# Kernel optimization log

Hardware: AMD Instinct MI355X
Metric: run time of the kernel (lower is better)

The kernel has to match this reference:

```python
import jax, jax.numpy as jnp
import numpy as np
import math

BS, SEQ, DIM, H, LK = 4, 4096, 768, 12, 256
HD = DIM // H  # 64
WIN = SEQ // LK  # 16, AdaptiveAvgPool1d reduces to uniform windows since SEQ % LK == 0


def setup_inputs() -> dict:
    key = jax.random.key(0)
    ks = jax.random.split(key, 12)
    s = 1.0 / math.sqrt(DIM)
    return {
        "query": jax.random.normal(ks[0], (BS, SEQ, DIM), jnp.float32),
        "key": jax.random.normal(ks[1], (BS, SEQ, DIM), jnp.float32),
        "value": jax.random.normal(ks[2], (BS, SEQ, DIM), jnp.float32),
        "mask": jax.random.normal(ks[3], (BS, SEQ), jnp.float32),  # mask<0 -> padded
        "Wq": jax.random.normal(ks[4], (DIM, DIM), jnp.float32) * s,
        "bq": jnp.zeros((DIM,), jnp.float32),
        "Wk": jax.random.normal(ks[5], (DIM, DIM), jnp.float32) * s,
        "bk": jnp.zeros((DIM,), jnp.float32),
        "Wv": jax.random.normal(ks[6], (DIM, DIM), jnp.float32) * s,
        "bv": jnp.zeros((DIM,), jnp.float32),
        "Wo": jax.random.normal(ks[7], (DIM, DIM), jnp.float32) * s,
        "bo": jnp.zeros((DIM,), jnp.float32),
    }


def reference(query, key, value, mask, Wq, bq, Wk, bk, Wv, bv, Wo, bo):
    bs, q_len, _ = query.shape
    # projections (nn.Linear: x @ W.T + b)
    Q = query @ Wq.T + bq
    K = key @ Wk.T + bk
    V = value @ Wv.T + bv
    # mask-fill padded K/V rows with 0 (mask dim==2 path: bool_mask = mask < 0)
    keep = (mask >= 0)[:, :, None]  # [bs, seq, 1]
    K = jnp.where(keep, K, 0.0)
    V = jnp.where(keep, V, 0.0)
    # adaptive avg pool over sequence -> linformer_k=256 (uniform windows of 16)
    Kc = K.reshape(bs, LK, WIN, DIM).mean(axis=2)  # [bs, 256, dim]
    Vc = V.reshape(bs, LK, WIN, DIM).mean(axis=2)
    # split heads
    Qh = Q.reshape(bs, q_len, H, HD) / math.sqrt(HD)  # scale fused
    Kh = Kc.reshape(bs, LK, H, HD)
    Vh = Vc.reshape(bs, LK, H, HD)
    # low-rank attention: [bs, h, q_len, 256]
    scores = jnp.einsum("bqhd,bkhd->bhqk", Qh, Kh)
    weights = jax.nn.softmax(scores, axis=-1)
    context = jnp.einsum("bhqk,bkhd->bqhd", weights, Vh).reshape(bs, q_len, DIM)
    return context @ Wo.T + bo
```

## Files before the change

### kernel.cpp

```cpp
#include <hip/hip_runtime.h>

#define BS_   4
#define SEQ_  4096
#define DIM_  768
#define NH_   12
#define HD_   64
#define LK_   256

typedef __attribute__((ext_vector_type(8))) short          bf8;
typedef __attribute__((ext_vector_type(8))) unsigned short us8;
typedef __attribute__((ext_vector_type(4))) float          f32x4;

typedef unsigned int u32g __attribute__((address_space(1)));
typedef unsigned int u32l __attribute__((address_space(3)));

#define LOG2E 1.44269504088896340736f

__device__ __forceinline__ unsigned short f2bf(float f) {
  unsigned u = __builtin_bit_cast(unsigned, f);
  u += 0x7fffu + ((u >> 16) & 1u);
  return (unsigned short)(u >> 16);
}

__device__ __forceinline__ us8 cvt8(const float* __restrict__ p) {
  const float4 a = *(const float4*)p;
  const float4 b = *(const float4*)(p + 4);
  us8 r;
  r[0] = f2bf(a.x); r[1] = f2bf(a.y); r[2] = f2bf(a.z); r[3] = f2bf(a.w);
  r[4] = f2bf(b.x); r[5] = f2bf(b.y); r[6] = f2bf(b.z); r[7] = f2bf(b.w);
  return r;
}

__global__ __launch_bounds__(256) void cvtbf_kernel(
    const float* __restrict__ query,
    const float* __restrict__ Wq, const float* __restrict__ Wk,
    const float* __restrict__ Wv, const float* __restrict__ Wo,
    unsigned short* __restrict__ Qbf, unsigned short* __restrict__ Wbf)
{
  const int i = blockIdx.x * 256 + threadIdx.x;
  const int QN8 = (BS_ * SEQ_ * DIM_) / 8;
  const int WN8 = (DIM_ * DIM_) / 8;
  if (i < QN8) { *(us8*)(Qbf + (size_t)i * 8) = cvt8(query + (size_t)i * 8); return; }
  int j = i - QN8;
  const float* src; unsigned short* dst;
  if      (j <     WN8) { src = Wq; dst = Wbf;                   }
  else if (j < 2 * WN8) { src = Wk; dst = Wbf + DIM_*DIM_;     j -=     WN8; }
  else if (j < 3 * WN8) { src = Wv; dst = Wbf + 2*DIM_*DIM_;   j -= 2 * WN8; }
  else if (j < 4 * WN8) { src = Wo; dst = Wbf + 3*DIM_*DIM_;   j -= 3 * WN8; }
  else return;
  *(us8*)(dst + (size_t)j * 8) = cvt8(src + (size_t)j * 8);
}

__global__ __launch_bounds__(256) void pool_kernel(
    const float* __restrict__ key, const float* __restrict__ value,
    const float* __restrict__ mask,
    unsigned short* __restrict__ pk, unsigned short* __restrict__ pv,
    float* __restrict__ frac)
{
  const int blk = blockIdx.x;
  const int b = blk >> 8;
  const int l = blk & 255;
  const int tid = threadIdx.x;
  __shared__ float keep[16];
  if (tid < 16) keep[tid] = (mask[b * SEQ_ + l * 16 + tid] >= 0.f) ? 1.f : 0.f;
  __syncthreads();
  float ak0 = 0.f, ak1 = 0.f, ak2 = 0.f, av0 = 0.f, av1 = 0.f, av2 = 0.f;
  #pragma unroll 1
  for (int w = 0; w < 16; ++w) {
    if (keep[w] != 0.f) {
      const size_t row = (size_t)(b * SEQ_ + l * 16 + w) * DIM_;
      const float* kr = key + row;
      const float* vr = value + row;
      ak0 += kr[tid]; ak1 += kr[tid + 256]; ak2 += kr[tid + 512];
      av0 += vr[tid]; av1 += vr[tid + 256]; av2 += vr[tid + 512];
    }
  }
  const size_t o = (size_t)(b * LK_ + l) * DIM_;
  const float s = 1.f / 16.f;
  pk[o + tid] = f2bf(ak0 * s); pk[o + tid + 256] = f2bf(ak1 * s); pk[o + tid + 512] = f2bf(ak2 * s);
  pv[o + tid] = f2bf(av0 * s); pv[o + tid + 256] = f2bf(av1 * s); pv[o + tid + 512] = f2bf(av2 * s);
  if (tid == 0) {
    float c = 0.f;
    for (int w = 0; w < 16; ++w) c += keep[w];
    frac[b * LK_ + l] = c * s;
  }
}

template<int SA, int SB, int MODE>
__global__ __launch_bounds__(256) void gemm_bt(
    const void* __restrict__ Aptr, const void* __restrict__ Bptr,
    const float* __restrict__ bias, const float* __restrict__ frac,
    void* __restrict__ Cout, int M, float scale)
{
  constexpr int K = DIM_;
  __shared__ __align__(16) unsigned short lA[128 * 32];
  __shared__ __align__(16) unsigned short lB[128 * 32];
  const int tid  = threadIdx.x;
  const int lane = tid & 63;
  const int wave = tid >> 6;
  const int brow = blockIdx.x * 128;
  const int bcol = blockIdx.y * 128;
  const int wr   = (wave >> 1) * 64;
  const int wc   = (wave & 1) * 64;
  const int fr   = lane & 15;
  const int fk   = (lane >> 4) * 8;

  f32x4 acc[4][4];
  #pragma unroll
  for (int i = 0; i < 4; ++i)
    #pragma unroll
    for (int j = 0; j < 4; ++j) acc[i][j] = (f32x4){0.f, 0.f, 0.f, 0.f};

  const int srow = tid >> 2;
  const int schk = (tid & 3) * 8;

  for (int k0 = 0; k0 < K; k0 += 32) {
    us8 a0, a1, b0, b1;
    if (SA == 1) {
      const float* A = (const float*)Aptr;
      a0 = cvt8(A + (size_t)(brow + srow) * K + k0 + schk);
      a1 = cvt8(A + (size_t)(brow + srow + 64) * K + k0 + schk);
    }
    if (SB == 1) {
      const float* B = (const float*)Bptr;
      b0 = cvt8(B + (size_t)(bcol + srow) * K + k0 + schk);
      b1 = cvt8(B + (size_t)(bcol + srow + 64) * K + k0 + schk);
    }
    __syncthreads();
    if (SA == 0) {
      const unsigned short* A = (const unsigned short*)Aptr;
      __builtin_amdgcn_global_load_lds(
          (const u32g*)(A + (size_t)(brow + srow) * K + k0 + schk),
          (u32l*)&lA[tid * 8], 16, 0, 0);
      __builtin_amdgcn_global_load_lds(
          (const u32g*)(A + (size_t)(brow + srow + 64) * K + k0 + schk),
          (u32l*)&lA[2048 + tid * 8], 16, 0, 0);
    } else {
      *(us8*)&lA[tid * 8]        = a0;
      *(us8*)&lA[2048 + tid * 8] = a1;
    }
    if (SB == 0) {
      const unsigned short* B = (const unsigned short*)Bptr;
      __builtin_amdgcn_global_load_lds(
          (const u32g*)(B + (size_t)(bcol + srow) * K + k0 + schk),
          (u32l*)&lB[tid * 8], 16, 0, 0);
      __builtin_amdgcn_global_load_lds(
          (const u32g*)(B + (size_t)(bcol + srow + 64) * K + k0 + schk),
          (u32l*)&lB[2048 + tid * 8], 16, 0, 0);
    } else {
      *(us8*)&lB[tid * 8]        = b0;
      *(us8*)&lB[2048 + tid * 8] = b1;
    }
    __syncthreads();
    bf8 af[4], bfv[4];
    #pragma unroll
    for (int mi = 0; mi < 4; ++mi)
      af[mi] = *(const bf8*)&lA[(wr + mi * 16 + fr) * 32 + fk];
    #pragma unroll
    for (int ni = 0; ni < 4; ++ni)
      bfv[ni] = *(const bf8*)&lB[(wc + ni * 16 + fr) * 32 + fk];
    #pragma unroll
    for (int mi = 0; mi < 4; ++mi)
      #pragma unroll
      for (int ni = 0; ni < 4; ++ni)
        acc[mi][ni] = __builtin_amdgcn_mfma_f32_16x16x32_bf16(af[mi], bfv[ni], acc[mi][ni], 0, 0, 0);
  }

  const int er = (lane >> 4) * 4;
  #pragma unroll
  for (int mi = 0; mi < 4; ++mi) {
    #pragma unroll
    for (int ni = 0; ni < 4; ++ni) {
      #pragma unroll
      for (int j = 0; j < 4; ++j) {
        const int r = brow + wr + mi * 16 + er + j;
        const int c = bcol + wc + ni * 16 + fr;
        float v = acc[mi][ni][j];
        if (MODE == 0) {
          v = (v + bias[c]) * scale;
          ((unsigned short*)Cout)[(size_t)r * DIM_ + c] = f2bf(v);
        } else if (MODE == 2) {
          ((float*)Cout)[(size_t)r * DIM_ + c] = v + bias[c];
        } else if (MODE == 3) {
          v += frac[r] * bias[c];
          const int bb = r >> 8, key = r & 255;
          const int hh = c >> 6, dd = c & 63;
          const int bh = bb * NH_ + hh;
          const size_t idx = (size_t)bh * 16384 +
              ((key >> 5) * 4 + (dd >> 4)) * 512 + ((key >> 3) & 3) * 128 +
              (dd & 15) * 8 + (key & 7);
          ((unsigned short*)Cout)[idx] = f2bf(v);
        } else {
          v += frac[r] * bias[c];
          const int bb = r >> 8, key = r & 255;
          const int hh = c >> 6, dd = c & 63;
          const int bh = bb * NH_ + hh;
          const int t = key >> 5, g = (key >> 3) & 3, sub = (key >> 2) & 1, jj = key & 3;
          const int frk = g * 4 + jj;
          const size_t idx = (size_t)bh * 16384 +
              (((t * 2 + sub) * 2) + (dd >> 5)) * 512 + ((dd >> 3) & 3) * 128 +
              frk * 8 + (dd & 7);
          ((unsigned short*)Cout)[idx] = f2bf(v);
        }
      }
    }
  }
}

__global__ __launch_bounds__(256) void attn_fused(
    const unsigned short* __restrict__ Qh,
    const unsigned short* __restrict__ Kf,
    const unsigned short* __restrict__ Vf,
    unsigned short* __restrict__ ctx)
{
  const int tid  = threadIdx.x;
  const int lane = tid & 63;
  const int wave = tid >> 6;
  const int bh = blockIdx.y;
  const int b = bh / NH_, h = bh % NH_;
  const int fr = lane & 15;
  const int hi = lane >> 4;
  const int qrow = blockIdx.x * 64 + wave * 16;

  const unsigned short* qp = Qh + (size_t)(b * SEQ_ + qrow + fr) * DIM_ + h * HD_ + hi * 8;
  const bf8 q0 = *(const bf8*)qp;
  const bf8 q1 = *(const bf8*)(qp + 32);

  const unsigned short* kb = Kf + (size_t)bh * 16384 + lane * 8;
  f32x4 scA[8], scB[8];
  #pragma unroll
  for (int s = 0; s < 8; ++s) {
    const bf8 ka0 = *(const bf8*)(kb + (s * 4 + 0) * 512);
    const bf8 ka1 = *(const bf8*)(kb + (s * 4 + 1) * 512);
    const bf8 kb0 = *(const bf8*)(kb + (s * 4 + 2) * 512);
    const bf8 kb1 = *(const bf8*)(kb + (s * 4 + 3) * 512);
    f32x4 x = (f32x4){0.f, 0.f, 0.f, 0.f};
    x = __builtin_amdgcn_mfma_f32_16x16x32_bf16(ka0, q0, x, 0, 0, 0);
    x = __builtin_amdgcn_mfma_f32_16x16x32_bf16(ka1, q1, x, 0, 0, 0);
    scA[s] = x;
    f32x4 y = (f32x4){0.f, 0.f, 0.f, 0.f};
    y = __builtin_amdgcn_mfma_f32_16x16x32_bf16(kb0, q0, y, 0, 0, 0);
    y = __builtin_amdgcn_mfma_f32_16x16x32_bf16(kb1, q1, y, 0, 0, 0);
    scB[s] = y;
  }

  float m = -1e30f;
  #pragma unroll
  for (int s = 0; s < 8; ++s)
    #pragma unroll
    for (int j = 0; j < 4; ++j) { m = fmaxf(m, scA[s][j]); m = fmaxf(m, scB[s][j]); }
  m = fmaxf(m, __shfl_xor(m, 16));
  m = fmaxf(m, __shfl_xor(m, 32));
  float sum = 0.f;
  #pragma unroll
  for (int s = 0; s < 8; ++s)
    #pragma unroll
    for (int j = 0; j < 4; ++j) {
      float pa = exp2f(scA[s][j] - m); scA[s][j] = pa; sum += pa;
      float pb = exp2f(scB[s][j] - m); scB[s][j] = pb; sum += pb;
    }
  sum += __shfl_xor(sum, 16);
  sum += __shfl_xor(sum, 32);
  const float inv = 1.f / sum;

  bf8 pa[8];
  #pragma unroll
  for (int s = 0; s < 8; ++s) {
    bf8 p;
    #pragma unroll
    for (int j = 0; j < 4; ++j) {
      p[j]     = (short)f2bf(scA[s][j] * inv);
      p[4 + j] = (short)f2bf(scB[s][j] * inv);
    }
    pa[s] = p;
  }

  const unsigned short* vb = Vf + (size_t)bh * 16384 + lane * 8;
  f32x4 acc[4];
  #pragma unroll
  for (int ct = 0; ct < 4; ++ct) acc[ct] = (f32x4){0.f, 0.f, 0.f, 0.f};
  #pragma unroll
  for (int s = 0; s < 8; ++s) {
    #pragma unroll
    for (int ct = 0; ct < 4; ++ct) {
      const bf8 vf = *(const bf8*)(vb + (s * 4 + ct) * 512);
      acc[ct] = __builtin_amdgcn_mfma_f32_16x16x32_bf16(pa[s], vf, acc[ct], 0, 0, 0);
    }
  }

  #pragma unroll
  for (int ct = 0; ct < 4; ++ct)
    #pragma unroll
    for (int j = 0; j < 4; ++j)
      ctx[(size_t)(b * SEQ_ + qrow + hi * 4 + j) * DIM_ + h * HD_ + ct * 16 + fr] =
          f2bf(acc[ct][j]);
}

extern "C" void kernel_launch(void* const* d_in, const int* in_sizes, int n_in,
                              void* d_out, int out_size, void* d_ws, size_t ws_size,
                              hipStream_t stream) {
  const float* query = (const float*)d_in[0];
  const float* key   = (const float*)d_in[1];
  const float* value = (const float*)d_in[2];
  const float* mask  = (const float*)d_in[3];
  const float* Wq    = (const float*)d_in[4];
  const float* bq    = (const float*)d_in[5];
  const float* Wk    = (const float*)d_in[6];
  const float* bk    = (const float*)d_in[7];
  const float* Wv    = (const float*)d_in[8];
  const float* bv    = (const float*)d_in[9];
  const float* Wo    = (const float*)d_in[10];
  const float* bo    = (const float*)d_in[11];
  float* out = (float*)d_out;

  char* ws = (char*)d_ws;
  unsigned short* Qh  = (unsigned short*)ws;
  unsigned short* ctx = (unsigned short*)(ws + 25165824);
  unsigned short* pK  = (unsigned short*)(ws + 50331648);
  unsigned short* pV  = (unsigned short*)(ws + 51904512);
  unsigned short* Kf  = (unsigned short*)(ws + 53477376);
  unsigned short* Vf  = (unsigned short*)(ws + 55050240);
  float*          frac = (float*)(ws + 56623104);
  unsigned short* Wbf = (unsigned short*)(ws + 56627200);
  const size_t NEED_BF = 56627200 + 4718592;

  const float qscale = 0.125f * LOG2E;

  pool_kernel<<<dim3(1024), dim3(256), 0, stream>>>(key, value, mask, pK, pV, frac);

  if (ws_size >= NEED_BF) {
    unsigned short* Qbf = ctx;
    cvtbf_kernel<<<dim3(7296), dim3(256), 0, stream>>>(query, Wq, Wk, Wv, Wo, Qbf, Wbf);
    gemm_bt<0, 0, 0><<<dim3(128, 6), dim3(256), 0, stream>>>(Qbf, Wbf,                 bq, nullptr, Qh, 16384, qscale);
    gemm_bt<0, 0, 4><<<dim3(8, 6),   dim3(256), 0, stream>>>(pK,  Wbf + DIM_*DIM_,     bk, frac,    Kf, 1024, 1.f);
    gemm_bt<0, 0, 3><<<dim3(8, 6),   dim3(256), 0, stream>>>(pV,  Wbf + 2*DIM_*DIM_,   bv, frac,    Vf, 1024, 1.f);
    attn_fused<<<dim3(64, 48), dim3(256), 0, stream>>>(Qh, Kf, Vf, ctx);
    gemm_bt<0, 0, 2><<<dim3(128, 6), dim3(256), 0, stream>>>(ctx, Wbf + 3*DIM_*DIM_,   bo, nullptr, out, 16384, 1.f);
  } else {
    gemm_bt<1, 1, 0><<<dim3(128, 6), dim3(256), 0, stream>>>(query, Wq, bq, nullptr, Qh, 16384, qscale);
    gemm_bt<0, 1, 4><<<dim3(8, 6),   dim3(256), 0, stream>>>(pK,    Wk, bk, frac,    Kf, 1024, 1.f);
    gemm_bt<0, 1, 3><<<dim3(8, 6),   dim3(256), 0, stream>>>(pV,    Wv, bv, frac,    Vf, 1024, 1.f);
    attn_fused<<<dim3(64, 48), dim3(256), 0, stream>>>(Qh, Kf, Vf, ctx);
    gemm_bt<0, 1, 2><<<dim3(128, 6), dim3(256), 0, stream>>>(ctx,   Wo, bo, nullptr, out, 16384, 1.f);
  }
}
```

Before: 155.4 us.

## Merge K/V projection launches, swizzle GEMM tiles, vectorize pooling, add MFMA priority hints

Several changes at once. The pooling kernel now uses 384 threads, each summing a float4 from either key or value, and writes packed bf16 stores. The K and V projection GEMMs are merged into one launch using blockIdx.z, which relies on pV and Vf sitting at fixed offsets after pK and Kf. The large GEMMs use a 1D grid with a block-index swizzle meant to improve L2 reuse. s_setprio hints are placed around the MFMA sections of attention, and the fp32-input fallback path is removed. These aim to cut launch count and memory inefficiency, but they depend on the workspace always being large enough.

```diff
diff --git a/kernel.cpp b/kernel.cpp
--- a/kernel.cpp
+++ b/kernel.cpp
@@ -9,6 +9,7 @@
 
 typedef __attribute__((ext_vector_type(8))) short          bf8;
 typedef __attribute__((ext_vector_type(8))) unsigned short us8;
+typedef __attribute__((ext_vector_type(4))) unsigned short us4;
 typedef __attribute__((ext_vector_type(4))) float          f32x4;
 
 typedef unsigned int u32g __attribute__((address_space(1)));
@@ -51,7 +52,7 @@
   *(us8*)(dst + (size_t)j * 8) = cvt8(src + (size_t)j * 8);
 }
 
-__global__ __launch_bounds__(256) void pool_kernel(
+__global__ __launch_bounds__(384) void pool_kernel(
     const float* __restrict__ key, const float* __restrict__ value,
     const float* __restrict__ mask,
     unsigned short* __restrict__ pk, unsigned short* __restrict__ pv,
@@ -64,33 +65,36 @@
   __shared__ float keep[16];
   if (tid < 16) keep[tid] = (mask[b * SEQ_ + l * 16 + tid] >= 0.f) ? 1.f : 0.f;
   __syncthreads();
-  float ak0 = 0.f, ak1 = 0.f, ak2 = 0.f, av0 = 0.f, av1 = 0.f, av2 = 0.f;
+  const int isV = tid >= 192;
+  const int c = isV ? tid - 192 : tid;
+  const float* src = isV ? value : key;
+  float4 acc = make_float4(0.f, 0.f, 0.f, 0.f);
   #pragma unroll 1
   for (int w = 0; w < 16; ++w) {
     if (keep[w] != 0.f) {
-      const size_t row = (size_t)(b * SEQ_ + l * 16 + w) * DIM_;
-      const float* kr = key + row;
-      const float* vr = value + row;
-      ak0 += kr[tid]; ak1 += kr[tid + 256]; ak2 += kr[tid + 512];
-      av0 += vr[tid]; av1 += vr[tid + 256]; av2 += vr[tid + 512];
-    }
-  }
-  const size_t o = (size_t)(b * LK_ + l) * DIM_;
+      const float4 v = *(const float4*)(src + (size_t)(b * SEQ_ + l * 16 + w) * DIM_ + c * 4);
+      acc.x += v.x; acc.y += v.y; acc.z += v.z; acc.w += v.w;
+    }
+  }
   const float s = 1.f / 16.f;
-  pk[o + tid] = f2bf(ak0 * s); pk[o + tid + 256] = f2bf(ak1 * s); pk[o + tid + 512] = f2bf(ak2 * s);
-  pv[o + tid] = f2bf(av0 * s); pv[o + tid + 256] = f2bf(av1 * s); pv[o + tid + 512] = f2bf(av2 * s);
+  unsigned short* dst = isV ? pv : pk;
+  us4 o4;
+  o4[0] = f2bf(acc.x * s); o4[1] = f2bf(acc.y * s);
+  o4[2] = f2bf(acc.z * s); o4[3] = f2bf(acc.w * s);
+  *(us4*)(dst + (size_t)(b * LK_ + l) * DIM_ + c * 4) = o4;
   if (tid == 0) {
-    float c = 0.f;
-    for (int w = 0; w < 16; ++w) c += keep[w];
-    frac[b * LK_ + l] = c * s;
-  }
-}
-
-template<int SA, int SB, int MODE>
+    float cnt = 0.f;
+    for (int w = 0; w < 16; ++w) cnt += keep[w];
+    frac[b * LK_ + l] = cnt * s;
+  }
+}
+
+template<int MODE, int SWZ>
 __global__ __launch_bounds__(256) void gemm_bt(
-    const void* __restrict__ Aptr, const void* __restrict__ Bptr,
-    const float* __restrict__ bias, const float* __restrict__ frac,
-    void* __restrict__ Cout, int M, float scale)
+    const void* __restrict__ Aptr_, const void* __restrict__ Bptr_,
+    const float* __restrict__ bias, const float* __restrict__ bias2,
+    const float* __restrict__ frac,
+    void* __restrict__ Cout, float scale)
 {
   constexpr int K = DIM_;
   __shared__ __align__(16) unsigned short lA[128 * 32];
@@ -98,8 +102,28 @@
   const int tid  = threadIdx.x;
   const int lane = tid & 63;
   const int wave = tid >> 6;
-  const int brow = blockIdx.x * 128;
-  const int bcol = blockIdx.y * 128;
+
+  int bx, by;
+  if (SWZ) {
+    const int r = (blockIdx.x & 7) * 96 + (blockIdx.x >> 3);
+    bx = r / 6; by = r % 6;
+  } else {
+    bx = blockIdx.x; by = blockIdx.y;
+  }
+  const int brow = bx * 128;
+  const int bcol = by * 128;
+
+  const unsigned short* A = (const unsigned short*)Aptr_;
+  const unsigned short* Bw = (const unsigned short*)Bptr_;
+  const float* bb = bias;
+  int isV = 0;
+  if (MODE == 34) {
+    isV = blockIdx.z;
+    A  += (size_t)isV * (BS_ * LK_ * DIM_);
+    Bw += (size_t)isV * (DIM_ * DIM_);
+    if (isV) bb = bias2;
+  }
+
   const int wr   = (wave >> 1) * 64;
   const int wc   = (wave & 1) * 64;
   const int fr   = lane & 15;
@@ -115,42 +139,19 @@
   const int schk = (tid & 3) * 8;
 
   for (int k0 = 0; k0 < K; k0 += 32) {
-    us8 a0, a1, b0, b1;
-    if (SA == 1) {
-      const float* A = (const float*)Aptr;
-      a0 = cvt8(A + (size_t)(brow + srow) * K + k0 + schk);
-      a1 = cvt8(A + (size_t)(brow + srow + 64) * K + k0 + schk);
-    }
-    if (SB == 1) {
-      const float* B = (const float*)Bptr;
-      b0 = cvt8(B + (size_t)(bcol + srow) * K + k0 + schk);
-      b1 = cvt8(B + (size_t)(bcol + srow + 64) * K + k0 + schk);
-    }
     __syncthreads();
-    if (SA == 0) {
-      const unsigned short* A = (const unsigned short*)Aptr;
-      __builtin_amdgcn_global_load_lds(
-          (const u32g*)(A + (size_t)(brow + srow) * K + k0 + schk),
-          (u32l*)&lA[tid * 8], 16, 0, 0);
-      __builtin_amdgcn_global_load_lds(
-          (const u32g*)(A + (size_t)(brow + srow + 64) * K + k0 + schk),
-          (u32l*)&lA[2048 + tid * 8], 16, 0, 0);
-    } else {
-      *(us8*)&lA[tid * 8]        = a0;
-      *(us8*)&lA[2048 + tid * 8] = a1;
-    }
-    if (SB == 0) {
-      const unsigned short* B = (const unsigned short*)Bptr;
-      __builtin_amdgcn_global_load_lds(
-          (const u32g*)(B + (size_t)(bcol + srow) * K + k0 + schk),
-          (u32l*)&lB[tid * 8], 16, 0, 0);
-      __builtin_amdgcn_global_load_lds(
-          (const u32g*)(B + (size_t)(bcol + srow + 64) * K + k0 + schk),
-          (u32l*)&lB[2048 + tid * 8], 16, 0, 0);
-    } else {
-      *(us8*)&lB[tid * 8]        = b0;
-      *(us8*)&lB[2048 + tid * 8] = b1;
-    }
+    __builtin_amdgcn_global_load_lds(
+        (const u32g*)(A + (size_t)(brow + srow) * K + k0 + schk),
+        (u32l*)&lA[tid * 8], 16, 0, 0);
+    __builtin_amdgcn_global_load_lds(
+        (const u32g*)(A + (size_t)(brow + srow + 64) * K + k0 + schk),
+        (u32l*)&lA[2048 + tid * 8], 16, 0, 0);
+    __builtin_amdgcn_global_load_lds(
+        (const u32g*)(Bw + (size_t)(bcol + srow) * K + k0 + schk),
+        (u32l*)&lB[tid * 8], 16, 0, 0);
+    __builtin_amdgcn_global_load_lds(
+        (const u32g*)(Bw + (size_t)(bcol + srow + 64) * K + k0 + schk),
+        (u32l*)&lB[2048 + tid * 8], 16, 0, 0);
     __syncthreads();
     bf8 af[4], bfv[4];
     #pragma unroll
@@ -181,25 +182,23 @@
           ((unsigned short*)Cout)[(size_t)r * DIM_ + c] = f2bf(v);
         } else if (MODE == 2) {
           ((float*)Cout)[(size_t)r * DIM_ + c] = v + bias[c];
-        } else if (MODE == 3) {
-          v += frac[r] * bias[c];
-          const int bb = r >> 8, key = r & 255;
+        } else {
+          v += frac[r] * bb[c];
+          const int bb_ = r >> 8, key = r & 255;
           const int hh = c >> 6, dd = c & 63;
-          const int bh = bb * NH_ + hh;
-          const size_t idx = (size_t)bh * 16384 +
-              ((key >> 5) * 4 + (dd >> 4)) * 512 + ((key >> 3) & 3) * 128 +
-              (dd & 15) * 8 + (key & 7);
-          ((unsigned short*)Cout)[idx] = f2bf(v);
-        } else {
-          v += frac[r] * bias[c];
-          const int bb = r >> 8, key = r & 255;
-          const int hh = c >> 6, dd = c & 63;
-          const int bh = bb * NH_ + hh;
-          const int t = key >> 5, g = (key >> 3) & 3, sub = (key >> 2) & 1, jj = key & 3;
-          const int frk = g * 4 + jj;
-          const size_t idx = (size_t)bh * 16384 +
-              (((t * 2 + sub) * 2) + (dd >> 5)) * 512 + ((dd >> 3) & 3) * 128 +
-              frk * 8 + (dd & 7);
+          const int bh = bb_ * NH_ + hh;
+          size_t idx;
+          if (isV) {
+            idx = (size_t)bh * 16384 +
+                ((key >> 5) * 4 + (dd >> 4)) * 512 + ((key >> 3) & 3) * 128 +
+                (dd & 15) * 8 + (key & 7) + 786432;
+          } else {
+            const int t = key >> 5, g = (key >> 3) & 3, sub = (key >> 2) & 1, jj = key & 3;
+            const int frk = g * 4 + jj;
+            idx = (size_t)bh * 16384 +
+                (((t * 2 + sub) * 2) + (dd >> 5)) * 512 + ((dd >> 3) & 3) * 128 +
+                frk * 8 + (dd & 7);
+          }
           ((unsigned short*)Cout)[idx] = f2bf(v);
         }
       }
@@ -228,6 +227,7 @@
 
   const unsigned short* kb = Kf + (size_t)bh * 16384 + lane * 8;
   f32x4 scA[8], scB[8];
+  __builtin_amdgcn_s_setprio(1);
   #pragma unroll
   for (int s = 0; s < 8; ++s) {
     const bf8 ka0 = *(const bf8*)(kb + (s * 4 + 0) * 512);
@@ -243,6 +243,7 @@
     y = __builtin_amdgcn_mfma_f32_16x16x32_bf16(kb1, q1, y, 0, 0, 0);
     scB[s] = y;
   }
+  __builtin_amdgcn_s_setprio(0);
 
   float m = -1e30f;
   #pragma unroll
@@ -256,8 +257,8 @@
   for (int s = 0; s < 8; ++s)
     #pragma unroll
     for (int j = 0; j < 4; ++j) {
-      float pa = exp2f(scA[s][j] - m); scA[s][j] = pa; sum += pa;
-      float pb = exp2f(scB[s][j] - m); scB[s][j] = pb; sum += pb;
+      const float pa = exp2f(scA[s][j] - m); scA[s][j] = pa; sum += pa;
+      const float pb = exp2f(scB[s][j] - m); scB[s][j] = pb; sum += pb;
     }
   sum += __shfl_xor(sum, 16);
   sum += __shfl_xor(sum, 32);
@@ -279,6 +280,7 @@
   f32x4 acc[4];
   #pragma unroll
   for (int ct = 0; ct < 4; ++ct) acc[ct] = (f32x4){0.f, 0.f, 0.f, 0.f};
+  __builtin_amdgcn_s_setprio(1);
   #pragma unroll
   for (int s = 0; s < 8; ++s) {
     #pragma unroll
@@ -287,6 +289,7 @@
       acc[ct] = __builtin_amdgcn_mfma_f32_16x16x32_bf16(pa[s], vf, acc[ct], 0, 0, 0);
     }
   }
+  __builtin_amdgcn_s_setprio(0);
 
   #pragma unroll
   for (int ct = 0; ct < 4; ++ct)
@@ -322,25 +325,17 @@
   unsigned short* Vf  = (unsigned short*)(ws + 55050240);
   float*          frac = (float*)(ws + 56623104);
   unsigned short* Wbf = (unsigned short*)(ws + 56627200);
-  const size_t NEED_BF = 56627200 + 4718592;
+  unsigned short* Qbf = ctx;
 
   const float qscale = 0.125f * LOG2E;
 
-  pool_kernel<<<dim3(1024), dim3(256), 0, stream>>>(key, value, mask, pK, pV, frac);
-
-  if (ws_size >= NEED_BF) {
-    unsigned short* Qbf = ctx;
-    cvtbf_kernel<<<dim3(7296), dim3(256), 0, stream>>>(query, Wq, Wk, Wv, Wo, Qbf, Wbf);
-    gemm_bt<0, 0, 0><<<dim3(128, 6), dim3(256), 0, stream>>>(Qbf, Wbf,                 bq, nullptr, Qh, 16384, qscale);
-    gemm_bt<0, 0, 4><<<dim3(8, 6),   dim3(256), 0, stream>>>(pK,  Wbf + DIM_*DIM_,     bk, frac,    Kf, 1024, 1.f);
-    gemm_bt<0, 0, 3><<<dim3(8, 6),   dim3(256), 0, stream>>>(pV,  Wbf + 2*DIM_*DIM_,   bv, frac,    Vf, 1024, 1.f);
-    attn_fused<<<dim3(64, 48), dim3(256), 0, stream>>>(Qh, Kf, Vf, ctx);
-    gemm_bt<0, 0, 2><<<dim3(128, 6), dim3(256), 0, stream>>>(ctx, Wbf + 3*DIM_*DIM_,   bo, nullptr, out, 16384, 1.f);
-  } else {
-    gemm_bt<1, 1, 0><<<dim3(128, 6), dim3(256), 0, stream>>>(query, Wq, bq, nullptr, Qh, 16384, qscale);
-    gemm_bt<0, 1, 4><<<dim3(8, 6),   dim3(256), 0, stream>>>(pK,    Wk, bk, frac,    Kf, 1024, 1.f);
-    gemm_bt<0, 1, 3><<<dim3(8, 6),   dim3(256), 0, stream>>>(pV,    Wv, bv, frac,    Vf, 1024, 1.f);
-    attn_fused<<<dim3(64, 48), dim3(256), 0, stream>>>(Qh, Kf, Vf, ctx);
-    gemm_bt<0, 1, 2><<<dim3(128, 6), dim3(256), 0, stream>>>(ctx,   Wo, bo, nullptr, out, 16384, 1.f);
-  }
-}
+  pool_kernel<<<dim3(1024), dim3(384), 0, stream>>>(key, value, mask, pK, pV, frac);
+  cvtbf_kernel<<<dim3(7296), dim3(256), 0, stream>>>(query, Wq, Wk, Wv, Wo, Qbf, Wbf);
+  gemm_bt<0, 1><<<dim3(768), dim3(256), 0, stream>>>(
+      Qbf, Wbf, bq, nullptr, nullptr, Qh, qscale);
+  gemm_bt<34, 0><<<dim3(8, 6, 2), dim3(256), 0, stream>>>(
+      pK, Wbf + DIM_*DIM_, bk, bv, frac, Kf, 1.f);
+  attn_fused<<<dim3(64, 48), dim3(256), 0, stream>>>(Qh, Kf, Vf, ctx);
+  gemm_bt<2, 1><<<dim3(768), dim3(256), 0, stream>>>(
+      ctx, Wbf + 3*DIM_*DIM_, bo, nullptr, nullptr, out, 1.f);
+}
```

Result: faster. 140.3 us (-9.7%).
